# Optimization experiments

Measured on AMD Instinct MI355X. Metric: run time of the kernel, lower is better.

The kernel has to match this reference:

```python
import jax, jax.numpy as jnp
import numpy as np

B, NB, L, K, C, H = 4, 256, 64, 65, 512, 8
HD = C // H
SCALE = HD ** -0.5


def setup_inputs() -> dict:
    key = jax.random.key(0)
    k = jax.random.split(key, 6)
    x = jax.random.normal(k[0], (B, NB * L, C), dtype=jnp.float32)
    mask = jax.random.bernoulli(k[1], 0.3, (NB, L, K))
    d = jnp.arange(L)
    mask = mask.at[:, d, d].set(True)      # self edges always on
    mask = mask.at[:, :, L].set(True)      # block-node column always on
    edge_feats = jax.random.normal(k[2], (NB, L, K, 4), dtype=jnp.float32)
    qkv_w = jax.random.normal(k[3], (C, 3 * C), dtype=jnp.float32) * (C ** -0.5)
    qkv_b = jnp.zeros((3 * C,), dtype=jnp.float32)
    proj_w = jax.random.normal(k[4], (C, C), dtype=jnp.float32) * (C ** -0.5)
    proj_b = jnp.zeros((C,), dtype=jnp.float32)
    return {"x": x, "attn_mask": mask, "edge_feats": edge_feats,
            "qkv_w": qkv_w, "qkv_b": qkv_b, "proj_w": proj_w, "proj_b": proj_b}


def reference(x, attn_mask, edge_feats, qkv_w, qkv_b, proj_w, proj_b):
    # x: (B, N, C) with N = NB*L (no padding needed); pool = 1, layout LxL+1
    x_blk = x.reshape(B, NB, L, C)                       # query tokens per leaf block
    block_node = x_blk.mean(axis=2, keepdims=True)       # (B, NB, 1, C)
    kv = jnp.concatenate([x_blk, block_node], axis=2)    # (B, NB, K, C), K = L+1

    qkv_q = x_blk @ qkv_w + qkv_b
    qkv_kv = kv @ qkv_w + qkv_b
    q = qkv_q[..., :C].reshape(B, NB, L, H, HD)
    k = qkv_kv[..., C:2 * C].reshape(B, NB, K, H, HD)
    v = qkv_kv[..., 2 * C:].reshape(B, NB, K, H, HD)

    scores = jnp.einsum('bnqhd,bnkhd->bnqkh', q, k) * SCALE  # (B,NB,L,K,H)

    # physics bias: edge_feats[..., :4] broadcast over batch; special/diagonal overrides
    bp = jnp.broadcast_to(edge_feats[None, ..., :4], (B, NB, L, K, 4))
    bp = bp.at[:, :, :, L, :].set(0.0)
    bp = bp.at[:, :, :, L, 3].set(1.0)                    # block-node key column
    d = jnp.arange(L)
    bp = bp.at[:, :, d, d, :].set(0.0)
    bp = bp.at[:, :, d, d, 3].set(1.0)                    # self edge
    scores = scores + bp[..., 3:4]                        # channel 3 additive bias (all heads)

    mask = attn_mask[None, :, :, :, None]                 # (1,NB,L,K,1)
    scores = jnp.where(mask, scores, jnp.float32(-1e9))
    attn = jax.nn.softmax(scores, axis=3)

    out = jnp.einsum('bnqkh,bnkhd->bnqhd', attn, v).reshape(B, NB * L, C)
    return out @ proj_w + proj_b
```

## Files before the change

### kernel.cpp

```cpp
#include <hip/hip_runtime.h>
#include <hip/hip_bf16.h>
#include <math.h>

typedef unsigned short u16;
typedef __attribute__((ext_vector_type(8))) short s16x8;
typedef __attribute__((ext_vector_type(4))) float f32x4;

#define NB_ 256
#define L_  64
#define KK_ 65
#define C_  512
#define H_  8
#define NEDGE (256*64*65)
#define MTOT  65536

__device__ __forceinline__ float b2f(u16 u){
  union { unsigned int i; float f; } x; x.i = ((unsigned int)u) << 16; return x.f;
}
__device__ __forceinline__ u16 f2b(float f){
  union { float f; unsigned int i; } x; x.f = f;
  return (u16)((x.i + 0x7FFFu + ((x.i >> 16) & 1u)) >> 16);
}

__device__ __forceinline__ void gload_lds16(const u16* g, u16* l){
  __builtin_amdgcn_global_load_lds(
      (const __attribute__((address_space(1))) unsigned int*)g,
      (__attribute__((address_space(3))) unsigned int*)l,
      16, 0, 0);
}

__global__ void detect_dtype_kernel(const u16* __restrict__ x, int* __restrict__ flagdt){
  __shared__ int cnt;
  if (threadIdx.x == 0) cnt = 0;
  __syncthreads();
  u16 v = x[(size_t)threadIdx.x * 2 * 1001];
  int e = (v >> 7) & 0xFF;
  if (e >= 141) atomicAdd(&cnt, 1);
  __syncthreads();
  if (threadIdx.x == 0) *flagdt = (cnt >= 8) ? 1 : 0;
}

__global__ void detect_mask_kernel(const unsigned char* __restrict__ m, int* __restrict__ flag){
  __shared__ int ok1, ok2, ok4;
  if (threadIdx.x == 0){ ok1 = 1; ok2 = 1; ok4 = 1; }
  __syncthreads();
  size_t e = (size_t)threadIdx.x * 65 + 64;
  if (((const unsigned char*)m)[e] == 0)  atomicAnd(&ok1, 0);
  if (((const unsigned short*)m)[e] == 0) atomicAnd(&ok2, 0);
  if (((const unsigned int*)m)[e] == 0u)  atomicAnd(&ok4, 0);
  __syncthreads();
  if (threadIdx.x == 0){
    int f = 4;
    if (ok2) f = 2;
    if (ok1) f = 1;
    *flag = f;
  }
}

__global__ void convert_kernel(const void* __restrict__ src, u16* __restrict__ dst,
                               long n, const int* __restrict__ flagdt){
  long i = ((long)blockIdx.x * 256 + threadIdx.x) * 8;
  if (i >= n) return;
  if (*flagdt){
    const float* s = (const float*)src + i;
    u16 o[8];
    #pragma unroll
    for (int j = 0; j < 8; ++j) o[j] = f2b(s[j]);
    *(s16x8*)(dst + i) = *(const s16x8*)o;
  } else {
    *(s16x8*)(dst + i) = *(const s16x8*)((const u16*)src + i);
  }
}

__global__ void build_bias_kernel(const void* __restrict__ edge,
                                  const unsigned char* __restrict__ mask,
                                  const int* __restrict__ flagdt,
                                  const int* __restrict__ flagm,
                                  u16* __restrict__ dst){
  long i = (long)blockIdx.x * 256 + threadIdx.x;
  if (i >= NEDGE) return;
  int kk = (int)(i % 65);
  long rowi = i / 65;
  int l = (int)(rowi & 63);
  int fm = *flagm;
  bool mt;
  if (fm == 1)      mt = mask[i] != 0;
  else if (fm == 2) mt = ((const unsigned short*)mask)[i] != 0;
  else              mt = ((const unsigned int*)mask)[i]   != 0u;
  float v;
  if (!mt)                      v = -1e9f;
  else if (kk == 64 || kk == l) v = 1.0f;
  else v = (*flagdt) ? ((const float*)edge)[i*4 + 3] : b2f(((const u16*)edge)[i*4 + 3]);
  dst[i] = f2b(v);
}

__global__ void transpose_conv_kernel(const void* __restrict__ in, u16* __restrict__ out,
                                      int R, int Cc, const int* __restrict__ flagdt){
  long i = (long)blockIdx.x * 256 + threadIdx.x;
  if (i < (long)R * Cc){
    int r = (int)(i / Cc), c = (int)(i % Cc);
    u16 v = (*flagdt) ? f2b(((const float*)in)[i]) : ((const u16*)in)[i];
    out[(long)c * R + r] = v;
  }
}

__global__ __launch_bounds__(256) void block_mean_kernel(const u16* __restrict__ x, u16* __restrict__ bm){
  int blk = blockIdx.x;
  const u16* xp = x + (long)blk * 64 * 512;
  for (int c = threadIdx.x; c < 512; c += 256){
    float s = 0.f;
    #pragma unroll
    for (int l = 0; l < 64; ++l) s += b2f(xp[l*512 + c]);
    bm[(long)blk * 512 + c] = f2b(s * 0.015625f);
  }
}

__global__ __launch_bounds__(256) void gemm_bt_kernel(
    const u16* __restrict__ A, const u16* __restrict__ BT,
    const u16* __restrict__ bias, u16* __restrict__ Cmat,
    int lda, int ldc, int Kdim, const int* __restrict__ flagdt, int out_mode,
    long row_off)
{
  __shared__ __align__(16) u16 As[2*128*32];
  __shared__ __align__(16) u16 Bs[2*128*32];
  const int t = threadIdx.x;
  const int lane = t & 63;
  const int w = t >> 6;
  const int wm = w & 1, wn = w >> 1;
  const int quad = lane >> 4;
  const int ml = lane & 15;

  const int nwg  = gridDim.x * gridDim.y;
  const int orig = blockIdx.y * gridDim.x + blockIdx.x;
  int lid = orig;
  if ((nwg & 7) == 0) lid = (orig & 7) * (nwg >> 3) + (orig >> 3);
  const int bx = lid % gridDim.x;
  const int by = lid / gridDim.x;
  const long colbase = (long)bx * 128;
  const long rowbase = (long)by * 128;
  const int of = out_mode ? *flagdt : 0;

  const f32x4 zero4 = {0.f, 0.f, 0.f, 0.f};
  f32x4 acc[4][4];
  #pragma unroll
  for (int i = 0; i < 4; ++i)
    #pragma unroll
    for (int j = 0; j < 4; ++j) acc[i][j] = zero4;

  const int c0 = t,       r0 = c0 >> 2, s0 = c0 & 3, g0 = s0 ^ ((r0 >> 1) & 3);
  const int c1 = t + 256, r1 = c1 >> 2, s1 = c1 & 3, g1 = s1 ^ ((r1 >> 1) & 3);
  const u16* Arow0 = A + (rowbase + r0) * (long)lda + g0*8;
  const u16* Arow1 = A + (rowbase + r1) * (long)lda + g1*8;
  const u16* Brow0 = BT + (colbase + r0) * (long)Kdim + g0*8;
  const u16* Brow1 = BT + (colbase + r1) * (long)Kdim + g1*8;

  for (int k0 = 0; k0 < Kdim; k0 += 64){
    __syncthreads();
    gload_lds16(Arow0 + k0,      As + w*512);
    gload_lds16(Arow1 + k0,      As + 2048 + w*512);
    gload_lds16(Arow0 + k0 + 32, As + 4096 + w*512);
    gload_lds16(Arow1 + k0 + 32, As + 4096 + 2048 + w*512);
    gload_lds16(Brow0 + k0,      Bs + w*512);
    gload_lds16(Brow1 + k0,      Bs + 2048 + w*512);
    gload_lds16(Brow0 + k0 + 32, Bs + 4096 + w*512);
    gload_lds16(Brow1 + k0 + 32, Bs + 4096 + 2048 + w*512);
    __syncthreads();
    #pragma unroll
    for (int hb = 0; hb < 2; ++hb){
      const u16* Ab = As + hb*4096;
      const u16* Bb = Bs + hb*4096;
      s16x8 af[4], bfr[4];
      #pragma unroll
      for (int i = 0; i < 4; ++i){
        int m = wm*64 + i*16 + ml;
        af[i]  = *(const s16x8*)(Ab + m*32 + ((quad ^ ((m>>1)&3)))*8);
        int n = wn*64 + i*16 + ml;
        bfr[i] = *(const s16x8*)(Bb + n*32 + ((quad ^ ((n>>1)&3)))*8);
      }
      #pragma unroll
      for (int i = 0; i < 4; ++i)
        #pragma unroll
        for (int j = 0; j < 4; ++j)
          acc[i][j] = __builtin_amdgcn_mfma_f32_16x16x32_bf16(af[i], bfr[j], acc[i][j], 0, 0, 0);
    }
  }

  #pragma unroll
  for (int j = 0; j < 4; ++j){
    long col = colbase + wn*64 + j*16 + ml;
    float bv = b2f(bias[col]);
    #pragma unroll
    for (int i = 0; i < 4; ++i){
      long row = row_off + rowbase + wm*64 + i*16 + quad*4;
      if (of){
        float* Cf = (float*)Cmat;
        #pragma unroll
        for (int r = 0; r < 4; ++r)
          Cf[(row + r) * (long)ldc + col] = acc[i][j][r] + bv;
      } else {
        #pragma unroll
        for (int r = 0; r < 4; ++r)
          Cmat[(row + r) * (long)ldc + col] = f2b(acc[i][j][r] + bv);
      }
    }
  }
}

__global__ __launch_bounds__(256, 4) void attn_kernel(
    const u16* __restrict__ Y, const u16* __restrict__ kvb,
    const u16* __restrict__ biasb, u16* __restrict__ AO)
{
  __shared__ __align__(16) u16 k_s [80*72];
  __shared__ __align__(16) u16 vT_s[64*104];
  __shared__ __align__(16) u16 P_s [64*104];

  const int t = threadIdx.x;
  const int lane = t & 63;
  const int w = t >> 6;
  const int quad = lane >> 4;
  const int ml = lane & 15;

  const int orig = blockIdx.y * gridDim.x + blockIdx.x;
  const int lid  = (orig & 7) * 256 + (orig >> 3);
  const int blk  = lid >> 1;
  const int hq   = lid & 1;
  const int nb = blk & (NB_ - 1);
  const long yrow0 = (long)blk * 64;

  float bb[5][4];
  #pragma unroll
  for (int j = 0; j < 5; ++j){
    int kk = j*16 + ml;
    #pragma unroll
    for (int r = 0; r < 4; ++r){
      int l = w*16 + quad*4 + r;
      bb[j][r] = (kk < 65) ? b2f(biasb[((long)nb*64 + l)*65 + kk]) : 0.f;
    }
  }

  for (int i = t; i < 64*31; i += 256){ int d = i/31, c = 65 + (i%31); vT_s[d*104 + c] = 0; }
  for (int i = t; i < 64*16; i += 256){ int l = i>>4,  c = 80 + (i&15); P_s[l*104 + c] = 0; }
  for (int i = t; i < 15*72; i += 256){ k_s[65*72 + i] = 0; }

  const int kk0 = t >> 3,  c8 = t & 7;
  const int kk1 = kk0 + 32;
  const u16* yb0 = Y + (yrow0 + kk0)*1536;
  const u16* yb1 = Y + (yrow0 + kk1)*1536;
  const u16* kvbase = kvb + (long)blk * 1024;

  const f32x4 zero4 = {0.f, 0.f, 0.f, 0.f};
  s16x8 kr0, vr0, kr1, vr1;

  for (int hh = 0; hh < 4; ++hh){
    const int h = hq*4 + hh;

    if (hh == 0){
      for (int c = t; c < 520; c += 256){
        int kk = c >> 3, cc = c & 7;
        const u16 *srck, *srcv;
        if (kk < 64){
          const u16* base = Y + (yrow0 + kk)*1536;
          srck = base + 512  + h*64 + cc*8;
          srcv = base + 1024 + h*64 + cc*8;
        } else {
          srck = kvbase + h*64 + cc*8;
          srcv = kvbase + 512 + h*64 + cc*8;
        }
        *(s16x8*)(k_s + kk*72 + cc*8) = *(const s16x8*)srck;
        s16x8 vv = *(const s16x8*)srcv;
        #pragma unroll
        for (int j = 0; j < 8; ++j){
          int jj = (j + cc) & 7;
          vT_s[(cc*8 + jj)*104 + kk] = (u16)vv[jj];
        }
      }
    } else {
      __syncthreads();
      *(s16x8*)(k_s + kk0*72 + c8*8) = kr0;
      *(s16x8*)(k_s + kk1*72 + c8*8) = kr1;
      #pragma unroll
      for (int j = 0; j < 8; ++j){
        int jj = (j + c8) & 7;
        vT_s[(c8*8 + jj)*104 + kk0] = (u16)vr0[jj];
        vT_s[(c8*8 + jj)*104 + kk1] = (u16)vr1[jj];
      }
      if (t < 8){
        *(s16x8*)(k_s + 64*72 + t*8) = *(const s16x8*)(kvbase + h*64 + t*8);
        s16x8 vv = *(const s16x8*)(kvbase + 512 + h*64 + t*8);
        #pragma unroll
        for (int j = 0; j < 8; ++j){
          int jj = (j + t) & 7;
          vT_s[(t*8 + jj)*104 + 64] = (u16)vv[jj];
        }
      }
    }
    __syncthreads();

    const u16* qrow = Y + (yrow0 + w*16 + ml)*1536 + h*64 + quad*8;
    s16x8 aq0 = *(const s16x8*)(qrow);
    s16x8 aq1 = *(const s16x8*)(qrow + 32);

    f32x4 sacc[5];
    #pragma unroll
    for (int j = 0; j < 5; ++j) sacc[j] = zero4;
    #pragma unroll
    for (int j = 0; j < 5; ++j){
      s16x8 bk0 = *(const s16x8*)(k_s + (j*16 + ml)*72 + quad*8);
      sacc[j] = __builtin_amdgcn_mfma_f32_16x16x32_bf16(aq0, bk0, sacc[j], 0, 0, 0);
      s16x8 bk1 = *(const s16x8*)(k_s + (j*16 + ml)*72 + 32 + quad*8);
      sacc[j] = __builtin_amdgcn_mfma_f32_16x16x32_bf16(aq1, bk1, sacc[j], 0, 0, 0);
    }

    if (hh < 3){
      const int hn = h + 1;
      kr0 = *(const s16x8*)(yb0 + 512  + hn*64 + c8*8);
      vr0 = *(const s16x8*)(yb0 + 1024 + hn*64 + c8*8);
      kr1 = *(const s16x8*)(yb1 + 512  + hn*64 + c8*8);
      vr1 = *(const s16x8*)(yb1 + 1024 + hn*64 + c8*8);
    }

    float sv[5][4];
    #pragma unroll
    for (int j = 0; j < 5; ++j){
      int kk = j*16 + ml;
      #pragma unroll
      for (int r = 0; r < 4; ++r)
        sv[j][r] = (kk < 65) ? (sacc[j][r]*0.125f + bb[j][r]) : -1e9f;
    }
    #pragma unroll
    for (int r = 0; r < 4; ++r){
      float mx = sv[0][r];
      #pragma unroll
      for (int j = 1; j < 5; ++j) mx = fmaxf(mx, sv[j][r]);
      #pragma unroll
      for (int o = 1; o < 16; o <<= 1) mx = fmaxf(mx, __shfl_xor(mx, o, 64));
      float sm = 0.f;
      #pragma unroll
      for (int j = 0; j < 5; ++j){ float e = __expf(sv[j][r] - mx); sv[j][r] = e; sm += e; }
      #pragma unroll
      for (int o = 1; o < 16; o <<= 1) sm += __shfl_xor(sm, o, 64);
      float inv = 1.0f / sm;
      #pragma unroll
      for (int j = 0; j < 5; ++j) sv[j][r] *= inv;
    }
    #pragma unroll
    for (int j = 0; j < 5; ++j){
      int kk = j*16 + ml;
      #pragma unroll
      for (int r = 0; r < 4; ++r)
        P_s[(w*16 + quad*4 + r)*104 + kk] = f2b(sv[j][r]);
    }
    __syncthreads();

    f32x4 oacc[4];
    #pragma unroll
    for (int j = 0; j < 4; ++j) oacc[j] = zero4;
    #pragma unroll
    for (int s = 0; s < 3; ++s){
      s16x8 ap = *(const s16x8*)(P_s + (w*16 + ml)*104 + s*32 + quad*8);
      #pragma unroll
      for (int j = 0; j < 4; ++j){
        s16x8 bv = *(const s16x8*)(vT_s + (j*16 + ml)*104 + s*32 + quad*8);
        oacc[j] = __builtin_amdgcn_mfma_f32_16x16x32_bf16(ap, bv, oacc[j], 0, 0, 0);
      }
    }
    #pragma unroll
    for (int j = 0; j < 4; ++j){
      int d = j*16 + ml;
      #pragma unroll
      for (int r = 0; r < 4; ++r){
        int l = w*16 + quad*4 + r;
        AO[(yrow0 + l)*512 + h*64 + d] = f2b(oacc[j][r]);
      }
    }
  }
}

extern "C" void kernel_launch(void* const* d_in, const int* in_sizes, int n_in,
                              void* d_out, int out_size, void* d_ws, size_t ws_size,
                              hipStream_t stream)
{
  const void* x_raw     = d_in[0];
  const unsigned char* mask = (const unsigned char*)d_in[1];
  const void* edge_raw  = d_in[2];
  const void* qkvw_raw  = d_in[3];
  const void* qkvb_raw  = d_in[4];
  const void* projw_raw = d_in[5];
  const void* projb_raw = d_in[6];

  char* ws = (char*)d_ws;
  size_t off = 0;
  int*  flagm  = (int*)ws;
  int*  flagdt = (int*)(ws + 4);         off += 1024;
  u16*  XC  = (u16*)(ws + off);          off += (size_t)33554432*2;
  u16*  EB  = (u16*)(ws + off);          off += (size_t)NEDGE*2;
  u16*  WT  = (u16*)(ws + off);          off += (size_t)1536*512*2;
  u16*  PT  = (u16*)(ws + off);          off += (size_t)512*512*2;
  u16*  QB  = (u16*)(ws + off);          off += 4096;
  u16*  PB  = (u16*)(ws + off);          off += 4096;
  u16*  BM  = (u16*)(ws + off);          off += (size_t)1024*512*2;
  u16*  KVB = (u16*)(ws + off);          off += (size_t)1024*1024*2;
  u16*  Y   = (u16*)(ws + off);          off += (size_t)MTOT*1536*2;
  u16*  AO  = (u16*)(ws + off);          off += (size_t)MTOT*512*2;

  detect_dtype_kernel<<<dim3(1), dim3(128), 0, stream>>>((const u16*)x_raw, flagdt);
  detect_mask_kernel<<<dim3(1), dim3(128), 0, stream>>>(mask, flagm);

  convert_kernel<<<dim3(33554432/8/256), dim3(256), 0, stream>>>(x_raw, XC, 33554432, flagdt);
  build_bias_kernel<<<dim3((NEDGE + 255)/256), dim3(256), 0, stream>>>(edge_raw, mask, flagdt, flagm, EB);
  transpose_conv_kernel<<<dim3((512*1536 + 255)/256), dim3(256), 0, stream>>>(qkvw_raw, WT, 512, 1536, flagdt);
  transpose_conv_kernel<<<dim3((512*512  + 255)/256), dim3(256), 0, stream>>>(projw_raw, PT, 512, 512, flagdt);
  convert_kernel<<<dim3(1), dim3(256), 0, stream>>>(qkvb_raw, QB, 1536, flagdt);
  convert_kernel<<<dim3(1), dim3(256), 0, stream>>>(projb_raw, PB, 512, flagdt);

  block_mean_kernel<<<dim3(1024), dim3(256), 0, stream>>>(XC, BM);
  gemm_bt_kernel<<<dim3(8, 8), dim3(256), 0, stream>>>(BM, WT + 512*512, QB + 512, KVB, 512, 1024, 512, flagdt, 0, 0);

  gemm_bt_kernel<<<dim3(12, MTOT/128), dim3(256), 0, stream>>>(XC, WT, QB, Y, 512, 1536, 512, flagdt, 0, 0);
  attn_kernel<<<dim3(1024, 2), dim3(256), 0, stream>>>(Y, KVB, EB, AO);
  gemm_bt_kernel<<<dim3(4, MTOT/128), dim3(256), 0, stream>>>(AO, PT, PB, (u16*)d_out, 512, 512, 512, flagdt, 1, 0);
}
```

Before: 559.0 us.

## Double-buffer GEMM LDS tiles to overlap global loads with MFMA compute

Replaces the single-buffer GEMM main loop, which loaded a 64-wide K slice and then computed with a barrier in between, with a two-buffer ping-pong over 32-wide K slices. The next slice is prefetched via global_load_lds while MFMAs run on the current buffer. LDS fragment reads move to inline-asm ds_read_b128 followed by an explicit lgkmcnt wait and a sched_barrier. The aim is to hide global-load latency behind matrix math. In exchange there are twice as many barriers per unit of K, and the inline asm limits what the compiler can schedule.

```diff
diff --git a/kernel.cpp b/kernel.cpp
--- a/kernel.cpp
+++ b/kernel.cpp
@@ -27,6 +27,14 @@
       (const __attribute__((address_space(1))) unsigned int*)g,
       (__attribute__((address_space(3))) unsigned int*)l,
       16, 0, 0);
+}
+
+__device__ __forceinline__ s16x8 ds_read128_asm(const u16* p){
+  s16x8 d;
+  unsigned a = (unsigned)(unsigned long long)
+      (const __attribute__((address_space(3))) u16*)p;
+  asm volatile("ds_read_b128 %0, %1" : "=v"(d) : "v"(a));
+  return d;
 }
 
 __global__ void detect_dtype_kernel(const u16* __restrict__ x, int* __restrict__ flagdt){
@@ -154,35 +162,46 @@
   const u16* Brow0 = BT + (colbase + r0) * (long)Kdim + g0*8;
   const u16* Brow1 = BT + (colbase + r1) * (long)Kdim + g1*8;
 
-  for (int k0 = 0; k0 < Kdim; k0 += 64){
-    __syncthreads();
-    gload_lds16(Arow0 + k0,      As + w*512);
-    gload_lds16(Arow1 + k0,      As + 2048 + w*512);
-    gload_lds16(Arow0 + k0 + 32, As + 4096 + w*512);
-    gload_lds16(Arow1 + k0 + 32, As + 4096 + 2048 + w*512);
-    gload_lds16(Brow0 + k0,      Bs + w*512);
-    gload_lds16(Brow1 + k0,      Bs + 2048 + w*512);
-    gload_lds16(Brow0 + k0 + 32, Bs + 4096 + w*512);
-    gload_lds16(Brow1 + k0 + 32, Bs + 4096 + 2048 + w*512);
-    __syncthreads();
-    #pragma unroll
-    for (int hb = 0; hb < 2; ++hb){
-      const u16* Ab = As + hb*4096;
-      const u16* Bb = Bs + hb*4096;
-      s16x8 af[4], bfr[4];
-      #pragma unroll
-      for (int i = 0; i < 4; ++i){
-        int m = wm*64 + i*16 + ml;
-        af[i]  = *(const s16x8*)(Ab + m*32 + ((quad ^ ((m>>1)&3)))*8);
-        int n = wn*64 + i*16 + ml;
-        bfr[i] = *(const s16x8*)(Bb + n*32 + ((quad ^ ((n>>1)&3)))*8);
-      }
-      #pragma unroll
-      for (int i = 0; i < 4; ++i)
-        #pragma unroll
-        for (int j = 0; j < 4; ++j)
-          acc[i][j] = __builtin_amdgcn_mfma_f32_16x16x32_bf16(af[i], bfr[j], acc[i][j], 0, 0, 0);
-    }
+  auto stage = [&](int b, int k0){
+    gload_lds16(Arow0 + k0, As + b*4096 + w*512);
+    gload_lds16(Arow1 + k0, As + b*4096 + 2048 + w*512);
+    gload_lds16(Brow0 + k0, Bs + b*4096 + w*512);
+    gload_lds16(Brow1 + k0, Bs + b*4096 + 2048 + w*512);
+  };
+  auto compute = [&](int b){
+    const u16* Ab = As + b*4096;
+    const u16* Bb = Bs + b*4096;
+    s16x8 af[4], bfr[4];
+    #pragma unroll
+    for (int i = 0; i < 4; ++i){
+      int m = wm*64 + i*16 + ml;
+      af[i]  = ds_read128_asm(Ab + m*32 + ((quad ^ ((m>>1)&3)))*8);
+      int n = wn*64 + i*16 + ml;
+      bfr[i] = ds_read128_asm(Bb + n*32 + ((quad ^ ((n>>1)&3)))*8);
+    }
+    asm volatile("s_waitcnt lgkmcnt(0)");
+    __builtin_amdgcn_sched_barrier(0);
+    #pragma unroll
+    for (int i = 0; i < 4; ++i)
+      #pragma unroll
+      for (int j = 0; j < 4; ++j)
+        acc[i][j] = __builtin_amdgcn_mfma_f32_16x16x32_bf16(af[i], bfr[j], acc[i][j], 0, 0, 0);
+  };
+  auto phase_end = [&](){
+    asm volatile("s_waitcnt vmcnt(0)" ::: "memory");
+    __builtin_amdgcn_s_barrier();
+  };
+
+  const int nk = Kdim >> 5;
+  stage(0, 0);
+  phase_end();
+  for (int kt = 0; kt < nk; kt += 2){
+    stage(1, (kt+1) << 5);
+    compute(0);
+    phase_end();
+    if (kt + 2 < nk) stage(0, (kt+2) << 5);
+    compute(1);
+    phase_end();
   }
 
   #pragma unroll
```

Result: slower. 573.0 us (+2.5%).

## Fuse block-mean into input conversion and append mean rows to main QKV GEMM

Applied to the files above, without the earlier changes.

The input conversion kernel now also computes each block's 64-row mean and writes it as extra rows after the token rows in the converted buffer. The separate block-mean kernel and the small KV GEMM are removed. The main QKV GEMM runs over the extended row count, and attention reads block-node K/V from the extra rows of Y. This saves a reread of the converted input and two launches, at the cost of computing an unused Q slice for the mean rows and a per-block reduction through shared memory.

```diff
diff --git a/kernel.cpp b/kernel.cpp
--- a/kernel.cpp
+++ b/kernel.cpp
@@ -13,6 +13,7 @@
 #define H_  8
 #define NEDGE (256*64*65)
 #define MTOT  65536
+#define MEXT  66560
 
 __device__ __forceinline__ float b2f(u16 u){
   union { unsigned int i; float f; } x; x.i = ((unsigned int)u) << 16; return x.f;
@@ -69,6 +70,43 @@
     *(s16x8*)(dst + i) = *(const s16x8*)o;
   } else {
     *(s16x8*)(dst + i) = *(const s16x8*)((const u16*)src + i);
+  }
+}
+
+__global__ __launch_bounds__(256) void convert_mean_kernel(
+    const void* __restrict__ src, u16* __restrict__ XC,
+    const int* __restrict__ flagdt){
+  __shared__ float ssum[4][512];
+  const int t  = threadIdx.x;
+  const int rg = t >> 6;
+  const int c8 = t & 63;
+  const int blk = blockIdx.x;
+  const int fdt = *flagdt;
+
+  float sum[8];
+  #pragma unroll
+  for (int j = 0; j < 8; ++j) sum[j] = 0.f;
+
+  for (int r = 0; r < 16; ++r){
+    long idx = ((long)blk*64 + rg*16 + r)*512 + c8*8;
+    u16 o[8];
+    if (fdt){
+      const float* s = (const float*)src + idx;
+      #pragma unroll
+      for (int j = 0; j < 8; ++j){ float v = s[j]; sum[j] += v; o[j] = f2b(v); }
+    } else {
+      s16x8 v = *(const s16x8*)((const u16*)src + idx);
+      #pragma unroll
+      for (int j = 0; j < 8; ++j){ u16 u = (u16)v[j]; sum[j] += b2f(u); o[j] = u; }
+    }
+    *(s16x8*)(XC + idx) = *(const s16x8*)o;
+  }
+  #pragma unroll
+  for (int j = 0; j < 8; ++j) ssum[rg][c8*8 + j] = sum[j];
+  __syncthreads();
+  for (int col = t; col < 512; col += 256){
+    float tot = ssum[0][col] + ssum[1][col] + ssum[2][col] + ssum[3][col];
+    XC[((long)MTOT + blk)*512 + col] = f2b(tot * 0.015625f);
   }
 }
 
@@ -104,17 +142,6 @@
   }
 }
 
-__global__ __launch_bounds__(256) void block_mean_kernel(const u16* __restrict__ x, u16* __restrict__ bm){
-  int blk = blockIdx.x;
-  const u16* xp = x + (long)blk * 64 * 512;
-  for (int c = threadIdx.x; c < 512; c += 256){
-    float s = 0.f;
-    #pragma unroll
-    for (int l = 0; l < 64; ++l) s += b2f(xp[l*512 + c]);
-    bm[(long)blk * 512 + c] = f2b(s * 0.015625f);
-  }
-}
-
 __global__ __launch_bounds__(256) void gemm_bt_kernel(
     const u16* __restrict__ A, const u16* __restrict__ BT,
     const u16* __restrict__ bias, u16* __restrict__ Cmat,
@@ -207,8 +234,8 @@
 }
 
 __global__ __launch_bounds__(256, 4) void attn_kernel(
-    const u16* __restrict__ Y, const u16* __restrict__ kvb,
-    const u16* __restrict__ biasb, u16* __restrict__ AO)
+    const u16* __restrict__ Y, const u16* __restrict__ biasb,
+    u16* __restrict__ AO)
 {
   __shared__ __align__(16) u16 k_s [80*72];
   __shared__ __align__(16) u16 vT_s[64*104];
@@ -246,7 +273,7 @@
   const int kk1 = kk0 + 32;
   const u16* yb0 = Y + (yrow0 + kk0)*1536;
   const u16* yb1 = Y + (yrow0 + kk1)*1536;
-  const u16* kvbase = kvb + (long)blk * 1024;
+  const u16* kvbase = Y + ((long)MTOT + blk)*1536;
 
   const f32x4 zero4 = {0.f, 0.f, 0.f, 0.f};
   s16x8 kr0, vr0, kr1, vr1;
@@ -263,8 +290,8 @@
           srck = base + 512  + h*64 + cc*8;
           srcv = base + 1024 + h*64 + cc*8;
         } else {
-          srck = kvbase + h*64 + cc*8;
-          srcv = kvbase + 512 + h*64 + cc*8;
+          srck = kvbase + 512  + h*64 + cc*8;
+          srcv = kvbase + 1024 + h*64 + cc*8;
         }
         *(s16x8*)(k_s + kk*72 + cc*8) = *(const s16x8*)srck;
         s16x8 vv = *(const s16x8*)srcv;
@@ -285,8 +312,8 @@
         vT_s[(c8*8 + jj)*104 + kk1] = (u16)vr1[jj];
       }
       if (t < 8){
-        *(s16x8*)(k_s + 64*72 + t*8) = *(const s16x8*)(kvbase + h*64 + t*8);
-        s16x8 vv = *(const s16x8*)(kvbase + 512 + h*64 + t*8);
+        *(s16x8*)(k_s + 64*72 + t*8) = *(const s16x8*)(kvbase + 512 + h*64 + t*8);
+        s16x8 vv = *(const s16x8*)(kvbase + 1024 + h*64 + t*8);
         #pragma unroll
         for (int j = 0; j < 8; ++j){
           int jj = (j + t) & 7;
@@ -392,31 +419,26 @@
   size_t off = 0;
   int*  flagm  = (int*)ws;
   int*  flagdt = (int*)(ws + 4);         off += 1024;
-  u16*  XC  = (u16*)(ws + off);          off += (size_t)33554432*2;
+  u16*  XC  = (u16*)(ws + off);          off += (size_t)MEXT*512*2;
   u16*  EB  = (u16*)(ws + off);          off += (size_t)NEDGE*2;
   u16*  WT  = (u16*)(ws + off);          off += (size_t)1536*512*2;
   u16*  PT  = (u16*)(ws + off);          off += (size_t)512*512*2;
   u16*  QB  = (u16*)(ws + off);          off += 4096;
   u16*  PB  = (u16*)(ws + off);          off += 4096;
-  u16*  BM  = (u16*)(ws + off);          off += (size_t)1024*512*2;
-  u16*  KVB = (u16*)(ws + off);          off += (size_t)1024*1024*2;
-  u16*  Y   = (u16*)(ws + off);          off += (size_t)MTOT*1536*2;
+  u16*  Y   = (u16*)(ws + off);          off += (size_t)MEXT*1536*2;
   u16*  AO  = (u16*)(ws + off);          off += (size_t)MTOT*512*2;
 
   detect_dtype_kernel<<<dim3(1), dim3(128), 0, stream>>>((const u16*)x_raw, flagdt);
   detect_mask_kernel<<<dim3(1), dim3(128), 0, stream>>>(mask, flagm);
 
-  convert_kernel<<<dim3(33554432/8/256), dim3(256), 0, stream>>>(x_raw, XC, 33554432, flagdt);
+  convert_mean_kernel<<<dim3(1024), dim3(256), 0, stream>>>(x_raw, XC, flagdt);
   build_bias_kernel<<<dim3((NEDGE + 255)/256), dim3(256), 0, stream>>>(edge_raw, mask, flagdt, flagm, EB);
   transpose_conv_kernel<<<dim3((512*1536 + 255)/256), dim3(256), 0, stream>>>(qkvw_raw, WT, 512, 1536, flagdt);
   transpose_conv_kernel<<<dim3((512*512  + 255)/256), dim3(256), 0, stream>>>(projw_raw, PT, 512, 512, flagdt);
   convert_kernel<<<dim3(1), dim3(256), 0, stream>>>(qkvb_raw, QB, 1536, flagdt);
   convert_kernel<<<dim3(1), dim3(256), 0, stream>>>(projb_raw, PB, 512, flagdt);
 
-  block_mean_kernel<<<dim3(1024), dim3(256), 0, stream>>>(XC, BM);
-  gemm_bt_kernel<<<dim3(8, 8), dim3(256), 0, stream>>>(BM, WT + 512*512, QB + 512, KVB, 512, 1024, 512, flagdt, 0, 0);
-
-  gemm_bt_kernel<<<dim3(12, MTOT/128), dim3(256), 0, stream>>>(XC, WT, QB, Y, 512, 1536, 512, flagdt, 0, 0);
-  attn_kernel<<<dim3(1024, 2), dim3(256), 0, stream>>>(Y, KVB, EB, AO);
+  gemm_bt_kernel<<<dim3(12, MEXT/128), dim3(256), 0, stream>>>(XC, WT, QB, Y, 512, 1536, 512, flagdt, 0, 0);
+  attn_kernel<<<dim3(1024, 2), dim3(256), 0, stream>>>(Y, EB, AO);
   gemm_bt_kernel<<<dim3(4, MTOT/128), dim3(256), 0, stream>>>(AO, PT, PB, (u16*)d_out, 512, 512, 512, flagdt, 1, 0);
 }
```

Result: slower. 579.9 us (+3.7%).
